# Optimization experiments

Measured on AMD Instinct MI355X. Metric: run time of the kernel, lower is better.

Reference implementation:

```python
import jax, jax.numpy as jnp
import numpy as np

B, T, C, H, N, L, V = 2, 512, 512, 8, 64, 12, 2560
DW, DA, DV, DG, F4 = 64, 64, 32, 128, 2048
GN_EPS = 64e-5  # torch GroupNorm eps = (1e-5)*head_size_divisor**2 with divisor 8


def _ln(x, w, b, eps=1e-5):
    m = x.mean(-1, keepdims=True)
    va = ((x - m) ** 2).mean(-1, keepdims=True)
    return (x - m) * jax.lax.rsqrt(va + eps) * w + b


def _group_norm(x, w, b):
    # GroupNorm(H groups) applied per token over each head's N channels
    xh = x.reshape(B, T, H, N)
    m = xh.mean(-1, keepdims=True)
    va = ((xh - m) ** 2).mean(-1, keepdims=True)
    return ((xh - m) * jax.lax.rsqrt(va + GN_EPS)).reshape(B, T, C) * w + b


def _time_shift(x):
    # ZeroPad2d((0,0,1,-1)): prepend zero step, drop last
    return jnp.pad(x, ((0, 0), (1, 0), (0, 0)))[:, :-1, :]


def _rwkv7_scan(r, w, k, v, a, b):
    # all inputs (B,T,H,N) float32; w already = exp(-exp(w_pre))
    def step(state, inp):
        r_t, w_t, k_t, v_t, a_t, b_t = inp  # (B,H,N)
        sa = jnp.einsum('bhij,bhj->bhi', state, a_t)  # S @ a (contract key dim)
        state = state * w_t[:, :, None, :] + sa[..., None] * b_t[:, :, None, :] + v_t[..., None] * k_t[:, :, None, :]
        return state, jnp.einsum('bhij,bhj->bhi', state, r_t)
    xs = tuple(jnp.moveaxis(t, 1, 0) for t in (r, w, k, v, a, b))  # (T,B,H,N)
    _, out = jax.lax.scan(step, jnp.zeros((B, H, N, N), jnp.float32), xs)
    return jnp.moveaxis(out, 0, 1)  # (B,T,H,N)


def _forward(tokens, emb, ln1_w, ln1_b, mx_r, mx_w, mx_k, mx_v, mx_a, mx_g,
             w0, w1, w2, a0, a1, a2, v0, v1, v2, g1, g2, k_k, k_a, r_k,
             Wr, Wk, Wv, Wo, gnx_w, gnx_b, ln2_w, ln2_b, Wfk, Wfv,
             lno_w, lno_b, Whead, bhead):
    hn = lambda t: t.reshape(B, T, H, N)
    x = emb[tokens]  # (B,T,C)
    v_first = x
    for i in range(L):
        # ---- RWKV-7 time-mix ----
        h = _ln(x, ln1_w[i], ln1_b[i])
        xx = _time_shift(h) - h
        xr = h + xx * mx_r[i]; xw = h + xx * mx_w[i]; xk = h + xx * mx_k[i]
        xv = h + xx * mx_v[i]; xa = h + xx * mx_a[i]; xg = h + xx * mx_g[i]
        r = xr @ Wr[i]
        wp = -jax.nn.softplus(-(w0[i] + jnp.tanh(xw @ w1[i]) @ w2[i])) - 0.5
        k = xk @ Wk[i]
        v = xv @ Wv[i]
        if i == 0:
            v_first = v
        else:
            v = v + (v_first - v) * jax.nn.sigmoid(v0[i] + (xv @ v1[i]) @ v2[i])
        a = jax.nn.sigmoid(a0[i] + (xa @ a1[i]) @ a2[i])
        g = jax.nn.sigmoid(xg @ g1[i]) @ g2[i]
        kk = hn(k * k_k[i])
        kk = (kk / jnp.maximum(jnp.linalg.norm(kk, axis=-1, keepdims=True), 1e-12)).reshape(B, T, C)
        k2 = k * (1.0 + (a - 1.0) * k_a[i])
        wdec = jnp.exp(-jnp.exp(wp.astype(jnp.float32)))
        y = _rwkv7_scan(hn(r).astype(jnp.float32), hn(wdec), hn(k2).astype(jnp.float32),
                        hn(v).astype(jnp.float32), hn(-kk).astype(jnp.float32),
                        hn(kk * a).astype(jnp.float32)).astype(x.dtype).reshape(B, T, C)
        y = _group_norm(y, gnx_w[i], gnx_b[i])
        y = y + ((hn(r) * hn(k2) * r_k[i].reshape(H, N)).sum(-1, keepdims=True) * hn(v)).reshape(B, T, C)
        x = x + (y * g) @ Wo[i]
        # ---- squared-ReLU channel-mix FFN (residual) ----
        h2 = _ln(x, ln2_w[i], ln2_b[i])
        x = x + jnp.square(jax.nn.relu(h2 @ Wfk[i])) @ Wfv[i]
    return _ln(x, lno_w, lno_b) @ Whead + bhead  # (B,T,V)


def setup_inputs():
    key = jax.random.key(0)
    ctr = [0]
    def nk():
        ctr[0] += 1
        return jax.random.fold_in(key, ctr[0])
    def nrm(shape, s=0.02):
        return jax.random.normal(nk(), shape, jnp.float32) * s
    def uni(shape):
        return jax.random.uniform(nk(), shape, dtype=jnp.float32)
    inp = {}
    inp['tokens'] = jax.random.randint(nk(), (B, T), 0, V, dtype=jnp.int32)
    inp['emb'] = nrm((V, C), 0.02)
    inp['ln1_w'] = jnp.ones((L, C)); inp['ln1_b'] = jnp.zeros((L, C))
    for nm in ('mx_r', 'mx_w', 'mx_k', 'mx_v', 'mx_a', 'mx_g'):
        inp[nm] = uni((L, C))
    inp['w0'] = nrm((L, C), 0.3) - 0.5
    inp['w1'] = nrm((L, C, DW)); inp['w2'] = nrm((L, DW, C), 0.1)
    inp['a0'] = nrm((L, C), 0.1); inp['a1'] = nrm((L, C, DA)); inp['a2'] = nrm((L, DA, C), 0.1)
    inp['v0'] = jnp.ones((L, C)); inp['v1'] = nrm((L, C, DV)); inp['v2'] = nrm((L, DV, C), 0.1)
    inp['g1'] = nrm((L, C, DG)); inp['g2'] = nrm((L, DG, C), 0.1)
    inp['k_k'] = 0.85 * jnp.ones((L, C)); inp['k_a'] = jnp.ones((L, C)); inp['r_k'] = nrm((L, C), 0.1)
    for nm in ('Wr', 'Wk', 'Wv', 'Wo'):
        inp[nm] = nrm((L, C, C), 0.02)
    inp['gnx_w'] = jnp.ones((L, C)); inp['gnx_b'] = jnp.zeros((L, C))
    inp['ln2_w'] = jnp.ones((L, C)); inp['ln2_b'] = jnp.zeros((L, C))
    inp['Wfk'] = nrm((L, C, F4), 0.02); inp['Wfv'] = nrm((L, F4, C), 0.02)
    inp['lno_w'] = jnp.ones((C,)); inp['lno_b'] = jnp.zeros((C,))
    inp['Whead'] = nrm((C, V), 0.02); inp['bhead'] = jnp.zeros((V,))
    return inp


def reference(tokens, emb, ln1_w, ln1_b, mx_r, mx_w, mx_k, mx_v, mx_a, mx_g,
              w0, w1, w2, a0, a1, a2, v0, v1, v2, g1, g2, k_k, k_a, r_k,
              Wr, Wk, Wv, Wo, gnx_w, gnx_b, ln2_w, ln2_b, Wfk, Wfv,
              lno_w, lno_b, Whead, bhead):
    return _forward(tokens, emb, ln1_w, ln1_b, mx_r, mx_w, mx_k, mx_v, mx_a, mx_g,
                    w0, w1, w2, a0, a1, a2, v0, v1, v2, g1, g2, k_k, k_a, r_k,
                    Wr, Wk, Wv, Wo, gnx_w, gnx_b, ln2_w, ln2_b, Wfk, Wfv,
                    lno_w, lno_b, Whead, bhead)
```

## Files before the change

### kernel.cpp

```cpp
#include <hip/hip_runtime.h>
#include <hip/hip_bf16.h>
#include <math.h>

#define Bq 2
#define Tq 512
#define Cq 512
#define Hq 8
#define Lq 12
#define Vq 2560
#define F4q 2048
#define BTq (Bq*Tq)

typedef float4 f4;
typedef __hip_bfloat16 bf16;
typedef __attribute__((ext_vector_type(8))) short bf16x8;
typedef __attribute__((ext_vector_type(4))) float f32x4;

static __device__ __forceinline__ float sigm(float x){ return 1.0f/(1.0f+expf(-x)); }
static __device__ __forceinline__ float splus(float x){ return fmaxf(x,0.0f) + log1pf(expf(-fabsf(x))); }
static __device__ __forceinline__ float b2f(short u){ unsigned int x = ((unsigned int)(unsigned short)u)<<16; float f; __builtin_memcpy(&f,&x,4); return f; }
static __device__ __forceinline__ short f2b(float f){ bf16 h = __float2bfloat16(f); unsigned short us; __builtin_memcpy(&us,&h,2); return (short)us; }

__device__ __forceinline__ void gload16(const void* gptr, void* lptr){
  __builtin_amdgcn_global_load_lds(
// ... 14 lines not shown
  int l = blockIdx.z;
  const float* s = src + (size_t)l*sstride;
  bf16* d = dst + (size_t)l*dstride;
  int n0 = blockIdx.x*32, k0 = blockIdx.y*32;
  int tx = threadIdx.x, ty = threadIdx.y;
  #pragma unroll
  for (int r=0;r<32;r+=8) tile[ty+r][tx] = s[(size_t)(k0+ty+r)*N + n0+tx];
  __syncthreads();
  #pragma unroll
  for (int r=0;r<32;r+=8) d[(size_t)(n0+ty+r)*K + k0+tx] = __float2bfloat16(tile[tx][ty+r]);
}

__global__ __launch_bounds__(256) void k_tr_split(const float* __restrict__ src,
    bf16* __restrict__ dhi, bf16* __restrict__ dlo,
    int K, int N, size_t sstride, size_t dstride){
  __shared__ float tile[32][33];
  int l = blockIdx.z;
  const float* s = src + (size_t)l*sstride;
  int n0 = blockIdx.x*32, k0 = blockIdx.y*32;
  int tx = threadIdx.x, ty = threadIdx.y;
  #pragma unroll
  for (int r=0;r<32;r+=8) tile[ty+r][tx] = s[(size_t)(k0+ty+r)*N + n0+tx];
  __syncthreads();
  #pragma unroll
  for (int r=0;r<32;r+=8){
    float v = tile[tx][ty+r];
    bf16 hv = __float2bfloat16(v);
    size_t idx = (size_t)l*dstride + (size_t)(n0+ty+r)*K + k0+tx;
    dhi[idx] = hv;
    dlo[idx] = __float2bfloat16(v - __bfloat162float(hv));
  }
}

__global__ __launch_bounds__(128) void k_ln(const float* __restrict__ x, const float* __restrict__ w,
    const float* __restrict__ b, float* __restrict__ o){
  int bt = blockIdx.x, tid = threadIdx.x;
  f4 v = ((const f4*)(x + (size_t)bt*Cq))[tid];
  float s = v.x+v.y+v.z+v.w;
  float q = v.x*v.x + v.y*v.y + v.z*v.z + v.w*v.w;
  #pragma unroll
  for (int m=1;m<64;m<<=1){ s += __shfl_xor(s,m); q += __shfl_xor(q,m); }
  __shared__ float ss[2], qs[2];
  if ((tid&63)==0){ ss[tid>>6]=s; qs[tid>>6]=q; }
  __syncthreads();
  s = ss[0]+ss[1]; q = qs[0]+qs[1];
  float mean = s*(1.0f/Cq);
  float inv = rsqrtf(q*(1.0f/Cq) - mean*mean + 1e-5f);
  f4 W = ((const f4*)w)[tid], Bb = ((const f4*)b)[tid];
  f4 r;
  r.x = (v.x-mean)*inv*W.x + Bb.x;
  r.y = (v.y-mean)*inv*W.y + Bb.y;
  r.z = (v.z-mean)*inv*W.z + Bb.z;
  r.w = (v.w-mean)*inv*W.w + Bb.w;
  ((f4*)(o + (size_t)bt*Cq))[tid] = r;
}

__global__ __launch_bounds__(128) void k_ln_split(const float* __restrict__ x, const float* __restrict__ w,
    const float* __restrict__ b, bf16* __restrict__ oh, bf16* __restrict__ ol){
  int bt = blockIdx.x, tid = threadIdx.x;
  f4 v = ((const f4*)(x + (size_t)bt*Cq))[tid];
  float s = v.x+v.y+v.z+v.w;
  float q = v.x*v.x + v.y*v.y + v.z*v.z + v.w*v.w;
  #pragma unroll
  for (int m=1;m<64;m<<=1){ s += __shfl_xor(s,m); q += __shfl_xor(q,m); }
  __shared__ float ss[2], qs[2];
  if ((tid&63)==0){ ss[tid>>6]=s; qs[tid>>6]=q; }
  __syncthreads();
  s = ss[0]+ss[1]; q = qs[0]+qs[1];
  float mean = s*(1.0f/Cq);
  float inv = rsqrtf(q*(1.0f/Cq) - mean*mean + 1e-5f);
  f4 W = ((const f4*)w)[tid], Bb = ((const f4*)b)[tid];
  float vv[4] = {(v.x-mean)*inv*W.x + Bb.x, (v.y-mean)*inv*W.y + Bb.y,
                 (v.z-mean)*inv*W.z + Bb.z, (v.w-mean)*inv*W.w + Bb.w};
  short4 hi, lo;
  short* hp = &hi.x; short* lp = &lo.x;
  #pragma unroll
  for (int u=0;u<4;u++){ hp[u] = f2b(vv[u]); lp[u] = f2b(vv[u] - b2f(hp[u])); }
  ((short4*)(oh + (size_t)bt*Cq))[tid] = hi;
  ((short4*)(ol + (size_t)bt*Cq))[tid] = lo;
}

__global__ __launch_bounds__(128) void k_ln_bf(const float* __restrict__ x, const float* __restrict__ w,
    const float* __restrict__ b, bf16* __restrict__ o){
  int bt = blockIdx.x, tid = threadIdx.x;
  f4 v = ((const f4*)(x + (size_t)bt*Cq))[tid];
  float s = v.x+v.y+v.z+v.w;
  float q = v.x*v.x + v.y*v.y + v.z*v.z + v.w*v.w;
  #pragma unroll
  for (int m=1;m<64;m<<=1){ s += __shfl_xor(s,m); q += __shfl_xor(q,m); }
  __shared__ float ss[2], qs[2];
  if ((tid&63)==0){ ss[tid>>6]=s; qs[tid>>6]=q; }
  __syncthreads();
  s = ss[0]+ss[1]; q = qs[0]+qs[1];
  float mean = s*(1.0f/Cq);
  float inv = rsqrtf(q*(1.0f/Cq) - mean*mean + 1e-5f);
  f4 W = ((const f4*)w)[tid], Bb = ((const f4*)b)[tid];
  short4 r;
  r.x = f2b((v.x-mean)*inv*W.x + Bb.x);
  r.y = f2b((v.y-mean)*inv*W.y + Bb.y);
  r.z = f2b((v.z-mean)*inv*W.z + Bb.z);
  r.w = f2b((v.w-mean)*inv*W.w + Bb.w);
  ((short4*)(o + (size_t)bt*Cq))[tid] = r;
}

__global__ __launch_bounds__(128) void k_mix_split(const float* __restrict__ h,
    const float* __restrict__ mr, const float* __restrict__ mw, const float* __restrict__ mk,
    const float* __restrict__ mv, const float* __restrict__ ma, const float* __restrict__ mg,
    bf16* __restrict__ xrh, bf16* __restrict__ xrl,
    bf16* __restrict__ xwh, bf16* __restrict__ xwl,
    bf16* __restrict__ xkh, bf16* __restrict__ xkl,
    bf16* __restrict__ xvh, bf16* __restrict__ xvl,
    bf16* __restrict__ xah, bf16* __restrict__ xal,
    bf16* __restrict__ xgh, bf16* __restrict__ xgl){
  int bt = blockIdx.x, tid = threadIdx.x;
  int t = bt & (Tq-1);
  f4 hc = ((const f4*)(h + (size_t)bt*Cq))[tid];
  f4 hp = make_float4(0.f,0.f,0.f,0.f);
  if (t) hp = ((const f4*)(h + (size_t)(bt-1)*Cq))[tid];
  float xxx = hp.x-hc.x, xxy = hp.y-hc.y, xxz = hp.z-hc.z, xxw = hp.w-hc.w;
  #define MIXS(dh, dl, m) { f4 M = ((const f4*)(m))[tid]; \
    float m0 = fmaf(xxx, M.x, hc.x), m1 = fmaf(xxy, M.y, hc.y); \
    float m2 = fmaf(xxz, M.z, hc.z), m3 = fmaf(xxw, M.w, hc.w); \
    short4 hi, lo; \
    hi.x = f2b(m0); lo.x = f2b(m0 - b2f(hi.x)); \
    hi.y = f2b(m1); lo.y = f2b(m1 - b2f(hi.y)); \
    hi.z = f2b(m2); lo.z = f2b(m2 - b2f(hi.z)); \
    hi.w = f2b(m3); lo.w = f2b(m3 - b2f(hi.w)); \
    ((short4*)((dh) + (size_t)bt*Cq))[tid] = hi; \
    ((short4*)((dl) + (size_t)bt*Cq))[tid] = lo; }
  MIXS(xrh, xrl, mr) MIXS(xwh, xwl, mw) MIXS(xkh, xkl, mk)
  MIXS(xvh, xvl, mv) MIXS(xah, xal, ma) MIXS(xgh, xgl, mg)
  #undef MIXS
}

template<int BM,int BN,int BK,int ACT,int OM>
__global__ __launch_bounds__(256) void k_sgemm(
    const bf16* __restrict__ Ah, const bf16* __restrict__ Al,
    const bf16* __restrict__ Bh, const bf16* __restrict__ Bl,
    void* __restrict__ Chv, bf16* __restrict__ Cl, int N, int K){
  constexpr int SWZ = (BK==64)?7:3;
  constexpr int ABYTES = BM*BK*2, BBYTES = BN*BK*2;
  __shared__ __align__(16) char lds[2][2*(ABYTES+BBYTES)];
  const int tid = threadIdx.x;
  const int w = tid>>6, ln = tid&63;
  const int wr = w>>1, wc = w&1;
  constexpr int WM = BM/2, WN = BN/2;
  constexpr int MR = WM/16, NR = WN/16;
  const int row0 = blockIdx.y*BM, col0 = blockIdx.x*BN;
  constexpr int LPR = BK/8;
  constexpr int RPC = 64/LPR;
  constexpr int CHA = BM/RPC, CHB = BN/RPC;
  const int srow = ln/LPR;
  const int kb  = (ln%LPR)*16;

  f32x4 acc[MR][NR];
  #pragma unroll
  for (int m=0;m<MR;m++)
    #pragma unroll
    for (int n=0;n<NR;n++)
      acc[m][n] = (f32x4){0.f,0.f,0.f,0.f};

  auto stage = [&](int buf, int k0){
    #pragma unroll
    for (int q=0;q<CHA/4;q++){
      int ch = w*(CHA/4)+q;
// ... 49 lines not shown
          acc[m][n] = __builtin_amdgcn_mfma_f32_16x16x32_bf16(ah[m], bh[n], acc[m][n], 0,0,0);
          acc[m][n] = __builtin_amdgcn_mfma_f32_16x16x32_bf16(ah[m], bl[n], acc[m][n], 0,0,0);
          acc[m][n] = __builtin_amdgcn_mfma_f32_16x16x32_bf16(al[m], bh[n], acc[m][n], 0,0,0);
        }
    }
    __syncthreads();
  }

  #pragma unroll
  for (int m=0;m<MR;m++){
    #pragma unroll
    for (int n=0;n<NR;n++){
      int col = col0 + wc*WN + n*16 + (ln&15);
      int rbase = row0 + wr*WM + m*16 + ((ln>>4)<<2);
      #pragma unroll
      for (int r=0;r<4;r++){
        float v = acc[m][n][r];
        if (ACT==1) v = tanhf(v);
        else if (ACT==2) v = sigm(v);
        else if (ACT==3){ v = fmaxf(v,0.f); v = v*v; }
        size_t o = (size_t)(rbase+r)*N + col;
        if (OM==0) ((float*)Chv)[o] = v;
        else if (OM==1) ((float*)Chv)[o] += v;
        else {
          bf16 hv = __float2bfloat16(v);
          ((bf16*)Chv)[o] = hv;
          Cl[o] = __float2bfloat16(v - __bfloat162float(hv));
        }
      }
    }
  }
}

template<int BM,int BN,int BK>
__global__ __launch_bounds__(256) void k_mgemm(const bf16* __restrict__ A,
    const bf16* __restrict__ Bt, const float* __restrict__ bias,
    float* __restrict__ Cm, int N, int K){
  constexpr int SWZ = (BK==64)?7:3;
  constexpr int ABYTES = BM*BK*2, BBYTES = BN*BK*2;
  __shared__ __align__(16) char lds[2][ABYTES+BBYTES];
  const int tid = threadIdx.x;
  const int w = tid>>6, ln = tid&63;
  const int wr = w>>1, wc = w&1;
  constexpr int WM = BM/2, WN = BN/2;
  constexpr int MR = WM/16, NR = WN/16;
  const int row0 = blockIdx.y*BM, col0 = blockIdx.x*BN;
  constexpr int LPR = BK/8;
  constexpr int RPC = 64/LPR;
  constexpr int CHA = BM/RPC, CHB = BN/RPC;
  const int srow = ln/LPR;
  const int kb  = (ln%LPR)*16;

  f32x4 acc[MR][NR];
  #pragma unroll
  for (int m=0;m<MR;m++)
    #pragma unroll
    for (int n=0;n<NR;n++)
      acc[m][n] = (f32x4){0.f,0.f,0.f,0.f};

  auto stage = [&](int buf, int k0){
    #pragma unroll
    for (int q=0;q<CHA/4;q++){
      int ch = w*(CHA/4)+q;
      int row = ch*RPC + srow;
      int kbs = kb ^ ((row&SWZ)<<4);
      gload16((const char*)(A + (size_t)(row0+row)*K + k0) + kbs, &lds[buf][ch*1024]);
// ... 56 lines not shown
    const float* __restrict__ vraw, const float* __restrict__ vfirst,
    const float* __restrict__ wpp, const float* __restrict__ aap, const float* __restrict__ vvp,
    const float* __restrict__ w0, const float* __restrict__ a0, const float* __restrict__ v0,
    const float* __restrict__ kkw, const float* __restrict__ kaw,
    float* __restrict__ scan_in, float* __restrict__ k2b, float* __restrict__ vb){
  int bt = blockIdx.x, hh = blockIdx.y, n = threadIdx.x;
  int c = (hh<<6) + n;
  size_t ic = (size_t)bt*Cq + c;
  int b = bt >> 9, t = bt & (Tq-1);
  float kvv = kb[ic];
  float kkq = kvv * kkw[c];
  float s = kkq*kkq;
  #pragma unroll
  for (int m=1;m<64;m<<=1) s += __shfl_xor(s,m);
  float kkn = kkq / fmaxf(sqrtf(s), 1e-12f);
  float aq = sigm(a0[c] + aap[ic]);
  float wvv = -splus(-(w0[c] + wpp[ic])) - 0.5f;
  float wd = expf(-expf(wvv));
  float vq;
  if (layer==0) vq = vfirst[ic];
  else { float vr = vraw[ic]; vq = fmaf(sigm(v0[c]+vvp[ic]), vfirst[ic]-vr, vr); }
  float k2q = kvv * fmaf(aq-1.0f, kaw[c], 1.0f);
  float* dst = scan_in + ((size_t)(b*Hq+hh)*Tq + t)*384;
  dst[n]       = rb[ic];
  dst[64+n]    = wd;
  dst[128+n]   = k2q;
  dst[192+n]   = vq;
  dst[256+n]   = -kkn;
  dst[320+n]   = kkn*aq;
  k2b[ic] = k2q;
  vb[ic]  = vq;
}

struct Step { float r[8], w[8], k[8], a[8], b[8], v; };

__device__ __forceinline__ void load_step(const float* __restrict__ st, int jc, int i, Step& s){
  *(f4*)&s.r[0] = *(const f4*)(st + jc);       *(f4*)&s.r[4] = *(const f4*)(st + jc + 4);
  *(f4*)&s.w[0] = *(const f4*)(st + 64 + jc);  *(f4*)&s.w[4] = *(const f4*)(st + 64 + jc + 4);
  *(f4*)&s.k[0] = *(const f4*)(st + 128 + jc); *(f4*)&s.k[4] = *(const f4*)(st + 128 + jc + 4);
  *(f4*)&s.a[0] = *(const f4*)(st + 256 + jc); *(f4*)&s.a[4] = *(const f4*)(st + 256 + jc + 4);
  *(f4*)&s.b[0] = *(const f4*)(st + 320 + jc); *(f4*)&s.b[4] = *(const f4*)(st + 320 + jc + 4);
  s.v = st[192 + i];
}

__device__ __forceinline__ float step_compute(float S[8], const Step& s){
  float sa0=0.f, sa1=0.f;
  #pragma unroll
  for (int u=0;u<4;u++){ sa0 = fmaf(S[u], s.a[u], sa0); sa1 = fmaf(S[u+4], s.a[u+4], sa1); }
  float sa = sa0+sa1;
  sa += __shfl_xor(sa,1); sa += __shfl_xor(sa,2); sa += __shfl_xor(sa,4);
  #pragma unroll
  for (int u=0;u<8;u++)
    S[u] = fmaf(s.v, s.k[u], fmaf(sa, s.b[u], S[u]*s.w[u]));
  float o0=0.f, o1=0.f;
  #pragma unroll
  for (int u=0;u<4;u++){ o0 = fmaf(S[u], s.r[u], o0); o1 = fmaf(S[u+4], s.r[u+4], o1); }
  float o = o0+o1;
  o += __shfl_xor(o,1); o += __shfl_xor(o,2); o += __shfl_xor(o,4);
  return o;
}

__global__ __launch_bounds__(64) void k_scan(const float* __restrict__ scan_in, float* __restrict__ y){
  int blk = blockIdx.x;
  int bh = blk>>3, w = blk&7;
  int lane = threadIdx.x;
  int il = lane>>3, c8 = lane&7, jc = c8<<3;
  int i = w*8 + il;
  int b = bh>>3, hh = bh&7;
  const float* base = scan_in + (size_t)bh*Tq*384;
  float* yrow = y + (size_t)b*Tq*Cq + (hh<<6) + i;
  float S[8];
  #pragma unroll
  for (int u=0;u<8;u++) S[u]=0.f;
  Step A_, B_;
  load_step(base, jc, i, A_);
  for (int t=0;t<Tq;t+=2){
    load_step(base + (size_t)(t+1)*384, jc, i, B_);
    float o = step_compute(S, A_);
    if (c8==0) yrow[(size_t)t*Cq] = o;
    if (t+2<Tq) load_step(base + (size_t)(t+2)*384, jc, i, A_);
    o = step_compute(S, B_);
    if (c8==0) yrow[(size_t)(t+1)*Cq] = o;
  }
}

__global__ __launch_bounds__(512) void k_post(const float* __restrict__ y,
    const float* __restrict__ rb, const float* __restrict__ k2b,
    const float* __restrict__ vb, const float* __restrict__ gb,
    const float* __restrict__ gnw, const float* __restrict__ gnb,
    const float* __restrict__ rk, bf16* __restrict__ zh, bf16* __restrict__ zl){
  int bt = blockIdx.x, c = threadIdx.x;
  size_t ic = (size_t)bt*Cq + c;
  float yv = y[ic];
  float s = yv, q = yv*yv;
  float rr = rb[ic]*k2b[ic]*rk[c];
  #pragma unroll
  for (int m=1;m<64;m<<=1){ s += __shfl_xor(s,m); q += __shfl_xor(q,m); rr += __shfl_xor(rr,m); }
  float mean = s*(1.0f/64.0f);
  float inv = rsqrtf(q*(1.0f/64.0f) - mean*mean + 64e-5f);
  float gn = (yv-mean)*inv*gnw[c] + gnb[c];
  float z = (gn + rr*vb[ic]) * gb[ic];
  bf16 hv = __float2bfloat16(z);
  zh[ic] = hv;
  zl[ic] = __float2bfloat16(z - __bfloat162float(hv));
}

extern "C" void kernel_launch(void* const* d_in, const int* in_sizes, int n_in,
                              void* d_out, int out_size, void* d_ws, size_t ws_size,
                              hipStream_t stream){
  const int*   tok  = (const int*)d_in[0];
  const float* emb  = (const float*)d_in[1];
  const float* ln1w = (const float*)d_in[2];
  const float* ln1b = (const float*)d_in[3];
  const float* mxr  = (const float*)d_in[4];
  const float* mxw  = (const float*)d_in[5];
// ... 5 lines not shown
  const float* w1   = (const float*)d_in[11];
  const float* w2   = (const float*)d_in[12];
  const float* a0   = (const float*)d_in[13];
  const float* a1   = (const float*)d_in[14];
  const float* a2   = (const float*)d_in[15];
  const float* v0   = (const float*)d_in[16];
  const float* v1   = (const float*)d_in[17];
  const float* v2   = (const float*)d_in[18];
  const float* g1   = (const float*)d_in[19];
  const float* g2   = (const float*)d_in[20];
  const float* kkw  = (const float*)d_in[21];
  const float* kaw  = (const float*)d_in[22];
  const float* rkw  = (const float*)d_in[23];
  const float* Wr   = (const float*)d_in[24];
  const float* Wk   = (const float*)d_in[25];
  const float* Wv   = (const float*)d_in[26];
  const float* Wo   = (const float*)d_in[27];
  const float* gnw  = (const float*)d_in[28];
  const float* gnb  = (const float*)d_in[29];
  const float* ln2w = (const float*)d_in[30];
  const float* ln2b = (const float*)d_in[31];
  const float* Wfk  = (const float*)d_in[32];
  const float* Wfv  = (const float*)d_in[33];
  const float* lnow = (const float*)d_in[34];
  const float* lnob = (const float*)d_in[35];
  const float* Whead= (const float*)d_in[36];
  const float* bhead= (const float*)d_in[37];
  float* out = (float*)d_out;

  float* ws = (float*)d_ws;
  size_t off = 0;
  const size_t BTC = (size_t)BTq*Cq;
  float* x      = ws + off; off += BTC;
  float* hf     = ws + off; off += BTC;
  float* rb     = ws + off; off += BTC;
  float* kb     = ws + off; off += BTC;
  float* vraw   = ws + off; off += BTC;
  float* vfirst = ws + off; off += BTC;
  float* wpp    = ws + off; off += BTC;
  float* aap    = ws + off; off += BTC;
  float* vvp    = ws + off; off += BTC;
  float* gbuf   = ws + off; off += BTC;
  float* k2b    = ws + off; off += BTC;
  float* vbuf   = ws + off; off += BTC;
  float* yb     = ws + off; off += BTC;
  float* scan_in= ws + off; off += (size_t)Bq*Hq*Tq*384;

  bf16* bp = (bf16*)(ws + off);
  size_t bo = 0;
  bf16* xrh = bp + bo; bo += BTC;  bf16* xrl = bp + bo; bo += BTC;
  bf16* xwh = bp + bo; bo += BTC;  bf16* xwl = bp + bo; bo += BTC;
  bf16* xkh = bp + bo; bo += BTC;  bf16* xkl = bp + bo; bo += BTC;
  bf16* xvh = bp + bo; bo += BTC;  bf16* xvl = bp + bo; bo += BTC;
  bf16* xah = bp + bo; bo += BTC;  bf16* xal = bp + bo; bo += BTC;
  bf16* xgh = bp + bo; bo += BTC;  bf16* xgl = bp + bo; bo += BTC;
  bf16* hh  = bp + bo; bo += BTC;  bf16* hl  = bp + bo; bo += BTC;
  bf16* zbh = bp + bo; bo += BTC;  bf16* zbl = bp + bo; bo += BTC;
  bf16* fkh = bp + bo; bo += (size_t)BTq*F4q;
  bf16* fkl = bp + bo; bo += (size_t)BTq*F4q;
  bf16* t1h = bp + bo; bo += (size_t)BTq*64;  bf16* t1l = bp + bo; bo += (size_t)BTq*64;
  bf16* t2h = bp + bo; bo += (size_t)BTq*64;  bf16* t2l = bp + bo; bo += (size_t)BTq*64;
  bf16* t3h = bp + bo; bo += (size_t)BTq*32;  bf16* t3l = bp + bo; bo += (size_t)BTq*32;
  bf16* t4h = bp + bo; bo += (size_t)BTq*128; bf16* t4l = bp + bo; bo += (size_t)BTq*128;
  const size_t CC = (size_t)Cq*Cq;
  bf16* WrTh = bp + bo; bo += Lq*CC;  bf16* WrTl = bp + bo; bo += Lq*CC;
  bf16* WkTh = bp + bo; bo += Lq*CC;  bf16* WkTl = bp + bo; bo += Lq*CC;
  bf16* WvTh = bp + bo; bo += Lq*CC;  bf16* WvTl = bp + bo; bo += Lq*CC;
  bf16* WoTh = bp + bo; bo += Lq*CC;  bf16* WoTl = bp + bo; bo += Lq*CC;
  const size_t C64 = (size_t)Cq*64, C32 = (size_t)Cq*32, C128 = (size_t)Cq*128;
  bf16* w1Th = bp + bo; bo += Lq*C64; bf16* w1Tl = bp + bo; bo += Lq*C64;
  bf16* w2Th = bp + bo; bo += Lq*C64; bf16* w2Tl = bp + bo; bo += Lq*C64;
  bf16* a1Th = bp + bo; bo += Lq*C64; bf16* a1Tl = bp + bo; bo += Lq*C64;
  bf16* a2Th = bp + bo; bo += Lq*C64; bf16* a2Tl = bp + bo; bo += Lq*C64;
  bf16* v1Th = bp + bo; bo += Lq*C32; bf16* v1Tl = bp + bo; bo += Lq*C32;
  bf16* v2Th = bp + bo; bo += Lq*C32; bf16* v2Tl = bp + bo; bo += Lq*C32;
  bf16* g1Th = bp + bo; bo += Lq*C128; bf16* g1Tl = bp + bo; bo += Lq*C128;
  bf16* g2Th = bp + bo; bo += Lq*C128; bf16* g2Tl = bp + bo; bo += Lq*C128;
  const size_t CF = (size_t)Cq*F4q;
  bf16* WfkTh = bp + bo; bo += CF;  bf16* WfkTl = bp + bo; bo += CF;
  bf16* WfvTh = bp + bo; bo += CF;  bf16* WfvTl = bp + bo; bo += CF;
  bf16* WhT   = bp + bo; bo += (size_t)Cq*Vq;

  dim3 tb(32,8);
  k_tr_split<<<dim3(16,16,Lq),tb,0,stream>>>(Wr, WrTh, WrTl, Cq, Cq, CC, CC);
  k_tr_split<<<dim3(16,16,Lq),tb,0,stream>>>(Wk, WkTh, WkTl, Cq, Cq, CC, CC);
  k_tr_split<<<dim3(16,16,Lq),tb,0,stream>>>(Wv, WvTh, WvTl, Cq, Cq, CC, CC);
  k_tr_split<<<dim3(16,16,Lq),tb,0,stream>>>(Wo, WoTh, WoTl, Cq, Cq, CC, CC);
  k_tr_split<<<dim3(2,16,Lq),tb,0,stream>>>(w1, w1Th, w1Tl, Cq, 64, C64, C64);
  k_tr_split<<<dim3(16,2,Lq),tb,0,stream>>>(w2, w2Th, w2Tl, 64, Cq, C64, C64);
  k_tr_split<<<dim3(2,16,Lq),tb,0,stream>>>(a1, a1Th, a1Tl, Cq, 64, C64, C64);
  k_tr_split<<<dim3(16,2,Lq),tb,0,stream>>>(a2, a2Th, a2Tl, 64, Cq, C64, C64);
  k_tr_split<<<dim3(1,16,Lq),tb,0,stream>>>(v1, v1Th, v1Tl, Cq, 32, C32, C32);
  k_tr_split<<<dim3(16,1,Lq),tb,0,stream>>>(v2, v2Th, v2Tl, 32, Cq, C32, C32);
  k_tr_split<<<dim3(4,16,Lq),tb,0,stream>>>(g1, g1Th, g1Tl, Cq, 128, C128, C128);
  k_tr_split<<<dim3(16,4,Lq),tb,0,stream>>>(g2, g2Th, g2Tl, 128, Cq, C128, C128);
  k_tr<<<dim3(80,16,1),tb,0,stream>>>(Whead, WhT, Cq, Vq, 0, 0);

  k_embed<<<BTq,128,0,stream>>>(tok, emb, x);

  dim3 gC(Cq/64, BTq/64);
  dim3 g64(1, BTq/64);
  dim3 g32(1, BTq/64);
  dim3 g128(2, BTq/64);
  dim3 gF(F4q/64, BTq/64);
  dim3 gH(Vq/64, BTq/64);

  for (int l=0;l<Lq;l++){
    size_t lc = (size_t)l*Cq;
    k_ln<<<BTq,128,0,stream>>>(x, ln1w+lc, ln1b+lc, hf);
    k_mix_split<<<BTq,128,0,stream>>>(hf, mxr+lc, mxw+lc, mxk+lc, mxv+lc, mxa+lc, mxg+lc,
                                      xrh,xrl, xwh,xwl, xkh,xkl, xvh,xvl, xah,xal, xgh,xgl);
    k_sgemm<64,64,64,0,0><<<gC,256,0,stream>>>(xrh, xrl, WrTh+l*CC, WrTl+l*CC, rb, nullptr, Cq, Cq);
    k_sgemm<64,64,64,0,0><<<gC,256,0,stream>>>(xkh, xkl, WkTh+l*CC, WkTl+l*CC, kb, nullptr, Cq, Cq);
    k_sgemm<64,64,64,0,0><<<gC,256,0,stream>>>(xvh, xvl, WvTh+l*CC, WvTl+l*CC,
                                               (l==0 ? vfirst : vraw), nullptr, Cq, Cq);
    k_sgemm<64,64,64,1,2><<<g64,256,0,stream>>>(xwh, xwl, w1Th+l*C64, w1Tl+l*C64, t1h, t1l, 64, Cq);
    k_sgemm<64,64,64,0,0><<<gC,256,0,stream>>>(t1h, t1l, w2Th+l*C64, w2Tl+l*C64, wpp, nullptr, Cq, 64);
    k_sgemm<64,64,64,0,2><<<g64,256,0,stream>>>(xah, xal, a1Th+l*C64, a1Tl+l*C64, t2h, t2l, 64, Cq);
    k_sgemm<64,64,64,0,0><<<gC,256,0,stream>>>(t2h, t2l, a2Th+l*C64, a2Tl+l*C64, aap, nullptr, Cq, 64);
    if (l > 0){
      k_sgemm<64,32,64,0,2><<<g32,256,0,stream>>>(xvh, xvl, v1Th+l*C32, v1Tl+l*C32, t3h, t3l, 32, Cq);
      k_sgemm<64,64,32,0,0><<<gC,256,0,stream>>>(t3h, t3l, v2Th+l*C32, v2Tl+l*C32, vvp, nullptr, Cq, 32);
    }
    k_sgemm<64,64,64,2,2><<<g128,256,0,stream>>>(xgh, xgl, g1Th+l*C128, g1Tl+l*C128, t4h, t4l, 128, Cq);
    k_sgemm<64,64,64,0,0><<<gC,256,0,stream>>>(t4h, t4l, g2Th+l*C128, g2Tl+l*C128, gbuf, nullptr, Cq, 128);
    k_prescan<<<dim3(BTq,Hq),64,0,stream>>>(l, rb, kb, vraw, vfirst, wpp, aap, vvp,
                                            w0+lc, a0+lc, v0+lc, kkw+lc, kaw+lc,
                                            scan_in, k2b, vbuf);
    k_scan<<<Bq*Hq*8,64,0,stream>>>(scan_in, yb);
    k_post<<<BTq,512,0,stream>>>(yb, rb, k2b, vbuf, gbuf, gnw+lc, gnb+lc, rkw+lc, zbh, zbl);
    k_sgemm<64,64,64,0,1><<<gC,256,0,stream>>>(zbh, zbl, WoTh+l*CC, WoTl+l*CC, x, nullptr, Cq, Cq);
    k_ln_split<<<BTq,128,0,stream>>>(x, ln2w+lc, ln2b+lc, hh, hl);
    k_tr_split<<<dim3(64,16,1),tb,0,stream>>>(Wfk + l*CF, WfkTh, WfkTl, Cq, F4q, 0, 0);
    k_tr_split<<<dim3(16,64,1),tb,0,stream>>>(Wfv + l*CF, WfvTh, WfvTl, F4q, Cq, 0, 0);
    k_sgemm<64,64,64,3,2><<<gF,256,0,stream>>>(hh, hl, WfkTh, WfkTl, fkh, fkl, F4q, Cq);
    k_sgemm<64,64,64,0,1><<<gC,256,0,stream>>>(fkh, fkl, WfvTh, WfvTl, x, nullptr, Cq, F4q);
  }
  k_ln_bf<<<BTq,128,0,stream>>>(x, lnow, lnob, hh);
  k_mgemm<64,64,64><<<gH,256,0,stream>>>(hh, WhT, bhead, out, Vq, Cq);
}
```

Before: 4.625 ms.

## Fuse LayerNorm with token mix, batch projection GEMMs, widen scan parallelism

Merges the first LayerNorm into the time-shift mix kernel. It recomputes the previous token's normalization so the intermediate fp32 buffer is no longer written and read back. The r/k/v projections and the two stages of LoRA-style low-rank GEMMs are grouped into three batched launches indexed by blockIdx.z, which cuts launch count and fills more CUs per launch. The scan kernel now splits each head's state over 16 blocks with 4 state columns per lane and a deeper prefetch, doubling the block count. The cost is a small amount of redundant LN work, padded wasted tiles in the grouped GEMMs, and the v1 low-rank GEMM now running on layer 0 too.

```diff
diff --git a/kernel.cpp b/kernel.cpp
--- a/kernel.cpp
+++ b/kernel.cpp
@@ -70,27 +70,59 @@
   }
 }
 
-__global__ __launch_bounds__(128) void k_ln(const float* __restrict__ x, const float* __restrict__ w,
-    const float* __restrict__ b, float* __restrict__ o){
+__global__ __launch_bounds__(128) void k_lnmix(const float* __restrict__ x,
+    const float* __restrict__ lw, const float* __restrict__ lb,
+    const float* __restrict__ mr, const float* __restrict__ mw, const float* __restrict__ mk,
+    const float* __restrict__ mv, const float* __restrict__ ma, const float* __restrict__ mg,
+    bf16* __restrict__ xrh, bf16* __restrict__ xrl,
+    bf16* __restrict__ xwh, bf16* __restrict__ xwl,
+    bf16* __restrict__ xkh, bf16* __restrict__ xkl,
+    bf16* __restrict__ xvh, bf16* __restrict__ xvl,
+    bf16* __restrict__ xah, bf16* __restrict__ xal,
+    bf16* __restrict__ xgh, bf16* __restrict__ xgl){
   int bt = blockIdx.x, tid = threadIdx.x;
-  f4 v = ((const f4*)(x + (size_t)bt*Cq))[tid];
-  float s = v.x+v.y+v.z+v.w;
-  float q = v.x*v.x + v.y*v.y + v.z*v.z + v.w*v.w;
-  #pragma unroll
-  for (int m=1;m<64;m<<=1){ s += __shfl_xor(s,m); q += __shfl_xor(q,m); }
-  __shared__ float ss[2], qs[2];
-  if ((tid&63)==0){ ss[tid>>6]=s; qs[tid>>6]=q; }
+  int t = bt & (Tq-1);
+  f4 vc = ((const f4*)(x + (size_t)bt*Cq))[tid];
+  f4 vp = make_float4(0.f,0.f,0.f,0.f);
+  if (t) vp = ((const f4*)(x + (size_t)(bt-1)*Cq))[tid];
+  float sc = vc.x+vc.y+vc.z+vc.w;
+  float qc = vc.x*vc.x+vc.y*vc.y+vc.z*vc.z+vc.w*vc.w;
+  float sp = vp.x+vp.y+vp.z+vp.w;
+  float qp = vp.x*vp.x+vp.y*vp.y+vp.z*vp.z+vp.w*vp.w;
+  #pragma unroll
+  for (int m=1;m<64;m<<=1){
+    sc += __shfl_xor(sc,m); qc += __shfl_xor(qc,m);
+    sp += __shfl_xor(sp,m); qp += __shfl_xor(qp,m);
+  }
+  __shared__ float sh[4][2];
+  if ((tid&63)==0){ int w=tid>>6; sh[0][w]=sc; sh[1][w]=qc; sh[2][w]=sp; sh[3][w]=qp; }
   __syncthreads();
-  s = ss[0]+ss[1]; q = qs[0]+qs[1];
-  float mean = s*(1.0f/Cq);
-  float inv = rsqrtf(q*(1.0f/Cq) - mean*mean + 1e-5f);
-  f4 W = ((const f4*)w)[tid], Bb = ((const f4*)b)[tid];
-  f4 r;
-  r.x = (v.x-mean)*inv*W.x + Bb.x;
-  r.y = (v.y-mean)*inv*W.y + Bb.y;
-  r.z = (v.z-mean)*inv*W.z + Bb.z;
-  r.w = (v.w-mean)*inv*W.w + Bb.w;
-  ((f4*)(o + (size_t)bt*Cq))[tid] = r;
+  sc = sh[0][0]+sh[0][1]; qc = sh[1][0]+sh[1][1];
+  sp = sh[2][0]+sh[2][1]; qp = sh[3][0]+sh[3][1];
+  float mc = sc*(1.0f/Cq), ic = rsqrtf(qc*(1.0f/Cq)-mc*mc+1e-5f);
+  float mp = sp*(1.0f/Cq), ip = rsqrtf(qp*(1.0f/Cq)-mp*mp+1e-5f);
+  f4 W = ((const f4*)lw)[tid], Bb = ((const f4*)lb)[tid];
+  float hcx = (vc.x-mc)*ic*W.x+Bb.x, hcy = (vc.y-mc)*ic*W.y+Bb.y;
+  float hcz = (vc.z-mc)*ic*W.z+Bb.z, hcw = (vc.w-mc)*ic*W.w+Bb.w;
+  float hpx=0.f, hpy=0.f, hpz=0.f, hpw=0.f;
+  if (t){
+    hpx = (vp.x-mp)*ip*W.x+Bb.x; hpy = (vp.y-mp)*ip*W.y+Bb.y;
+    hpz = (vp.z-mp)*ip*W.z+Bb.z; hpw = (vp.w-mp)*ip*W.w+Bb.w;
+  }
+  float xxx = hpx-hcx, xxy = hpy-hcy, xxz = hpz-hcz, xxw = hpw-hcw;
+  #define MIXS(dh, dl, m) { f4 M = ((const f4*)(m))[tid]; \
+    float m0 = fmaf(xxx, M.x, hcx), m1 = fmaf(xxy, M.y, hcy); \
+    float m2 = fmaf(xxz, M.z, hcz), m3 = fmaf(xxw, M.w, hcw); \
+    short4 hi, lo; \
+    hi.x = f2b(m0); lo.x = f2b(m0 - b2f(hi.x)); \
+    hi.y = f2b(m1); lo.y = f2b(m1 - b2f(hi.y)); \
+    hi.z = f2b(m2); lo.z = f2b(m2 - b2f(hi.z)); \
+    hi.w = f2b(m3); lo.w = f2b(m3 - b2f(hi.w)); \
+    ((short4*)((dh) + (size_t)bt*Cq))[tid] = hi; \
+    ((short4*)((dl) + (size_t)bt*Cq))[tid] = lo; }
+  MIXS(xrh, xrl, mr) MIXS(xwh, xwl, mw) MIXS(xkh, xkl, mk)
+  MIXS(xvh, xvl, mv) MIXS(xah, xal, ma) MIXS(xgh, xgl, mg)
+  #undef MIXS
 }
 
 __global__ __launch_bounds__(128) void k_ln_split(const float* __restrict__ x, const float* __restrict__ w,
@@ -139,36 +171,6 @@
   r.z = f2b((v.z-mean)*inv*W.z + Bb.z);
   r.w = f2b((v.w-mean)*inv*W.w + Bb.w);
   ((short4*)(o + (size_t)bt*Cq))[tid] = r;
-}
-
-__global__ __launch_bounds__(128) void k_mix_split(const float* __restrict__ h,
-    const float* __restrict__ mr, const float* __restrict__ mw, const float* __restrict__ mk,
-    const float* __restrict__ mv, const float* __restrict__ ma, const float* __restrict__ mg,
-    bf16* __restrict__ xrh, bf16* __restrict__ xrl,
-    bf16* __restrict__ xwh, bf16* __restrict__ xwl,
-    bf16* __restrict__ xkh, bf16* __restrict__ xkl,
-    bf16* __restrict__ xvh, bf16* __restrict__ xvl,
-    bf16* __restrict__ xah, bf16* __restrict__ xal,
-    bf16* __restrict__ xgh, bf16* __restrict__ xgl){
-  int bt = blockIdx.x, tid = threadIdx.x;
-  int t = bt & (Tq-1);
-  f4 hc = ((const f4*)(h + (size_t)bt*Cq))[tid];
-  f4 hp = make_float4(0.f,0.f,0.f,0.f);
-  if (t) hp = ((const f4*)(h + (size_t)(bt-1)*Cq))[tid];
-  float xxx = hp.x-hc.x, xxy = hp.y-hc.y, xxz = hp.z-hc.z, xxw = hp.w-hc.w;
-  #define MIXS(dh, dl, m) { f4 M = ((const f4*)(m))[tid]; \
-    float m0 = fmaf(xxx, M.x, hc.x), m1 = fmaf(xxy, M.y, hc.y); \
-    float m2 = fmaf(xxz, M.z, hc.z), m3 = fmaf(xxw, M.w, hc.w); \
-    short4 hi, lo; \
-    hi.x = f2b(m0); lo.x = f2b(m0 - b2f(hi.x)); \
-    hi.y = f2b(m1); lo.y = f2b(m1 - b2f(hi.y)); \
-    hi.z = f2b(m2); lo.z = f2b(m2 - b2f(hi.z)); \
-    hi.w = f2b(m3); lo.w = f2b(m3 - b2f(hi.w)); \
-    ((short4*)((dh) + (size_t)bt*Cq))[tid] = hi; \
-    ((short4*)((dl) + (size_t)bt*Cq))[tid] = lo; }
-  MIXS(xrh, xrl, mr) MIXS(xwh, xwl, mw) MIXS(xkh, xkl, mk)
-  MIXS(xvh, xvl, mv) MIXS(xah, xal, ma) MIXS(xgh, xgl, mg)
-  #undef MIXS
 }
 
 template<int BM,int BN,int BK,int ACT,int OM>
@@ -284,6 +286,134 @@
   }
 }
 
+struct SBatch {
+  const bf16* Ah[4]; const bf16* Al[4];
+  const bf16* Bh[4]; const bf16* Bl[4];
+  void* Ch[4]; bf16* Cl[4];
+  int N[4]; int K[4]; int act[4];
+};
+
+template<int BM,int BN,int BK,int OM>
+__global__ __launch_bounds__(256) void k_sgemm_b(SBatch p){
+  const int z = blockIdx.z;
+  const int N = p.N[z], K = p.K[z], act = p.act[z];
+  const int col0 = blockIdx.x*BN;
+  if (col0 >= N) return;
+  const bf16* __restrict__ Ah = p.Ah[z];
+  const bf16* __restrict__ Al = p.Al[z];
+  const bf16* __restrict__ Bh = p.Bh[z];
+  const bf16* __restrict__ Bl = p.Bl[z];
+  void* Chv = p.Ch[z];
+  bf16* Cl = p.Cl[z];
+  constexpr int SWZ = (BK==64)?7:3;
+  constexpr int ABYTES = BM*BK*2, BBYTES = BN*BK*2;
+  __shared__ __align__(16) char lds[2][2*(ABYTES+BBYTES)];
+  const int tid = threadIdx.x;
+  const int w = tid>>6, ln = tid&63;
+  const int wr = w>>1, wc = w&1;
+  constexpr int WM = BM/2, WN = BN/2;
+  constexpr int MR = WM/16, NR = WN/16;
+  const int row0 = blockIdx.y*BM;
+  constexpr int LPR = BK/8;
+  constexpr int RPC = 64/LPR;
+  constexpr int CHA = BM/RPC, CHB = BN/RPC;
+  const int srow = ln/LPR;
+  const int kb  = (ln%LPR)*16;
+
+  f32x4 acc[MR][NR];
+  #pragma unroll
+  for (int m=0;m<MR;m++)
+    #pragma unroll
+    for (int n=0;n<NR;n++)
+      acc[m][n] = (f32x4){0.f,0.f,0.f,0.f};
+
+  auto stage = [&](int buf, int k0){
+    #pragma unroll
+    for (int q=0;q<CHA/4;q++){
+      int ch = w*(CHA/4)+q;
+      int row = ch*RPC + srow;
+      int kbs = kb ^ ((row&SWZ)<<4);
+      size_t go = (size_t)(row0+row)*K + k0;
+      gload16((const char*)(Ah+go)+kbs, &lds[buf][ch*1024]);
+      gload16((const char*)(Al+go)+kbs, &lds[buf][ABYTES + ch*1024]);
+    }
+    #pragma unroll
+    for (int q=0;q<CHB/4;q++){
+      int ch = w*(CHB/4)+q;
+      int row = ch*RPC + srow;
+      int kbs = kb ^ ((row&SWZ)<<4);
+      size_t go = (size_t)(col0+row)*K + k0;
+      gload16((const char*)(Bh+go)+kbs, &lds[buf][2*ABYTES + ch*1024]);
+      gload16((const char*)(Bl+go)+kbs, &lds[buf][2*ABYTES+BBYTES + ch*1024]);
+    }
+  };
+
+  stage(0, 0);
+  __syncthreads();
+  const int nt = K/BK;
+  for (int t=0;t<nt;t++){
+    int buf = t&1;
+    if (t+1<nt) stage(buf^1, (t+1)*BK);
+    const char* Lah = &lds[buf][0];
+    const char* Lal = &lds[buf][ABYTES];
+    const char* Lbh = &lds[buf][2*ABYTES];
+    const char* Lbl = &lds[buf][2*ABYTES+BBYTES];
+    #pragma unroll
+    for (int kk=0;kk<BK/32;kk++){
+      bf16x8 ah[MR], al[MR], bh[NR], bl[NR];
+      int klo = kk*64 + ((ln>>4)<<4);
+      #pragma unroll
+      for (int m=0;m<MR;m++){
+        int row = wr*WM + m*16 + (ln&15);
+        int off = row*(BK*2) + (klo ^ ((row&SWZ)<<4));
+        ah[m] = *(const bf16x8*)(Lah + off);
+        al[m] = *(const bf16x8*)(Lal + off);
+      }
+      #pragma unroll
+      for (int n=0;n<NR;n++){
+        int row = wc*WN + n*16 + (ln&15);
+        int off = row*(BK*2) + (klo ^ ((row&SWZ)<<4));
+        bh[n] = *(const bf16x8*)(Lbh + off);
+        bl[n] = *(const bf16x8*)(Lbl + off);
+      }
+      #pragma unroll
+      for (int m=0;m<MR;m++)
+        #pragma unroll
+        for (int n=0;n<NR;n++){
+          acc[m][n] = __builtin_amdgcn_mfma_f32_16x16x32_bf16(ah[m], bh[n], acc[m][n], 0,0,0);
+          acc[m][n] = __builtin_amdgcn_mfma_f32_16x16x32_bf16(ah[m], bl[n], acc[m][n], 0,0,0);
+          acc[m][n] = __builtin_amdgcn_mfma_f32_16x16x32_bf16(al[m], bh[n], acc[m][n], 0,0,0);
+        }
+    }
+    __syncthreads();
+  }
+
+  #pragma unroll
+  for (int m=0;m<MR;m++){
+    #pragma unroll
+    for (int n=0;n<NR;n++){
+      int col = col0 + wc*WN + n*16 + (ln&15);
+      if (col >= N) continue;
+      int rbase = row0 + wr*WM + m*16 + ((ln>>4)<<2);
+      #pragma unroll
+      for (int r=0;r<4;r++){
+        float v = acc[m][n][r];
+        if (act==1) v = tanhf(v);
+        else if (act==2) v = sigm(v);
+        else if (act==3){ v = fmaxf(v,0.f); v = v*v; }
+        size_t o = (size_t)(rbase+r)*N + col;
+        if (OM==0) ((float*)Chv)[o] = v;
+        else if (OM==1) ((float*)Chv)[o] += v;
+        else {
+          bf16 hv = __float2bfloat16(v);
+          ((bf16*)Chv)[o] = hv;
+          Cl[o] = __float2bfloat16(v - __bfloat162float(hv));
+        }
+      }
+    }
+  }
+}
+
 template<int BM,int BN,int BK>
 __global__ __launch_bounds__(256) void k_mgemm(const bf16* __restrict__ A,
     const bf16* __restrict__ Bt, const float* __restrict__ bias,
@@ -406,55 +536,61 @@
   vb[ic]  = vq;
 }
 
-struct Step { float r[8], w[8], k[8], a[8], b[8], v; };
-
-__device__ __forceinline__ void load_step(const float* __restrict__ st, int jc, int i, Step& s){
-  *(f4*)&s.r[0] = *(const f4*)(st + jc);       *(f4*)&s.r[4] = *(const f4*)(st + jc + 4);
-  *(f4*)&s.w[0] = *(const f4*)(st + 64 + jc);  *(f4*)&s.w[4] = *(const f4*)(st + 64 + jc + 4);
-  *(f4*)&s.k[0] = *(const f4*)(st + 128 + jc); *(f4*)&s.k[4] = *(const f4*)(st + 128 + jc + 4);
-  *(f4*)&s.a[0] = *(const f4*)(st + 256 + jc); *(f4*)&s.a[4] = *(const f4*)(st + 256 + jc + 4);
-  *(f4*)&s.b[0] = *(const f4*)(st + 320 + jc); *(f4*)&s.b[4] = *(const f4*)(st + 320 + jc + 4);
+struct Step4 { float r[4], w[4], k[4], a[4], b[4], v; };
+
+__device__ __forceinline__ void load_step4(const float* __restrict__ st, int jc, int i, Step4& s){
+  *(f4*)&s.r[0] = *(const f4*)(st + jc);
+  *(f4*)&s.w[0] = *(const f4*)(st + 64 + jc);
+  *(f4*)&s.k[0] = *(const f4*)(st + 128 + jc);
+  *(f4*)&s.a[0] = *(const f4*)(st + 256 + jc);
+  *(f4*)&s.b[0] = *(const f4*)(st + 320 + jc);
   s.v = st[192 + i];
 }
 
-__device__ __forceinline__ float step_compute(float S[8], const Step& s){
-  float sa0=0.f, sa1=0.f;
-  #pragma unroll
-  for (int u=0;u<4;u++){ sa0 = fmaf(S[u], s.a[u], sa0); sa1 = fmaf(S[u+4], s.a[u+4], sa1); }
-  float sa = sa0+sa1;
-  sa += __shfl_xor(sa,1); sa += __shfl_xor(sa,2); sa += __shfl_xor(sa,4);
-  #pragma unroll
-  for (int u=0;u<8;u++)
+__device__ __forceinline__ float step_compute4(float S[4], const Step4& s){
+  float sa = 0.f;
+  #pragma unroll
+  for (int u=0;u<4;u++) sa = fmaf(S[u], s.a[u], sa);
+  sa += __shfl_xor(sa,1); sa += __shfl_xor(sa,2);
+  sa += __shfl_xor(sa,4); sa += __shfl_xor(sa,8);
+  #pragma unroll
+  for (int u=0;u<4;u++)
     S[u] = fmaf(s.v, s.k[u], fmaf(sa, s.b[u], S[u]*s.w[u]));
-  float o0=0.f, o1=0.f;
-  #pragma unroll
-  for (int u=0;u<4;u++){ o0 = fmaf(S[u], s.r[u], o0); o1 = fmaf(S[u+4], s.r[u+4], o1); }
-  float o = o0+o1;
-  o += __shfl_xor(o,1); o += __shfl_xor(o,2); o += __shfl_xor(o,4);
+  float o = 0.f;
+  #pragma unroll
+  for (int u=0;u<4;u++) o = fmaf(S[u], s.r[u], o);
+  o += __shfl_xor(o,1); o += __shfl_xor(o,2);
+  o += __shfl_xor(o,4); o += __shfl_xor(o,8);
   return o;
 }
 
 __global__ __launch_bounds__(64) void k_scan(const float* __restrict__ scan_in, float* __restrict__ y){
   int blk = blockIdx.x;
-  int bh = blk>>3, w = blk&7;
+  int bh = blk>>4, w = blk&15;
   int lane = threadIdx.x;
-  int il = lane>>3, c8 = lane&7, jc = c8<<3;
-  int i = w*8 + il;
+  int il = lane>>4, c16 = lane&15, jc = c16<<2;
+  int i = w*4 + il;
   int b = bh>>3, hh = bh&7;
   const float* base = scan_in + (size_t)bh*Tq*384;
   float* yrow = y + (size_t)b*Tq*Cq + (hh<<6) + i;
-  float S[8];
-  #pragma unroll
-  for (int u=0;u<8;u++) S[u]=0.f;
-  Step A_, B_;
-  load_step(base, jc, i, A_);
-  for (int t=0;t<Tq;t+=2){
-    load_step(base + (size_t)(t+1)*384, jc, i, B_);
-    float o = step_compute(S, A_);
-    if (c8==0) yrow[(size_t)t*Cq] = o;
-    if (t+2<Tq) load_step(base + (size_t)(t+2)*384, jc, i, A_);
-    o = step_compute(S, B_);
-    if (c8==0) yrow[(size_t)(t+1)*Cq] = o;
+  float S[4] = {0.f,0.f,0.f,0.f};
+  Step4 P0,P1,P2,P3;
+  load_step4(base,      jc,i,P0);
+  load_step4(base+384,  jc,i,P1);
+  load_step4(base+768,  jc,i,P2);
+  for (int t=0;t<Tq;t+=4){
+    if (t+3<Tq) load_step4(base+(size_t)(t+3)*384, jc,i,P3);
+    float o = step_compute4(S,P0);
+    if (c16==0) yrow[(size_t)t*Cq] = o;
+    if (t+4<Tq) load_step4(base+(size_t)(t+4)*384, jc,i,P0);
+    o = step_compute4(S,P1);
+    if (c16==0) yrow[(size_t)(t+1)*Cq] = o;
+    if (t+5<Tq) load_step4(base+(size_t)(t+5)*384, jc,i,P1);
+    o = step_compute4(S,P2);
+    if (c16==0) yrow[(size_t)(t+2)*Cq] = o;
+    if (t+6<Tq) load_step4(base+(size_t)(t+6)*384, jc,i,P2);
+    o = step_compute4(S,P3);
+    if (c16==0) yrow[(size_t)(t+3)*Cq] = o;
   }
 }
 
@@ -526,7 +662,6 @@
   size_t off = 0;
   const size_t BTC = (size_t)BTq*Cq;
   float* x      = ws + off; off += BTC;
-  float* hf     = ws + off; off += BTC;
   float* rb     = ws + off; off += BTC;
   float* kb     = ws + off; off += BTC;
   float* vraw   = ws + off; off += BTC;
@@ -566,7 +701,7 @@
   bf16* w2Th = bp + bo; bo += Lq*C64; bf16* w2Tl = bp + bo; bo += Lq*C64;
   bf16* a1Th = bp + bo; bo += Lq*C64; bf16* a1Tl = bp + bo; bo += Lq*C64;
   bf16* a2Th = bp + bo; bo += Lq*C64; bf16* a2Tl = bp + bo; bo += Lq*C64;
-  bf16* v1Th = bp + bo; bo += Lq*C32; bf16* v1Tl = bp + bo; bo += Lq*C32;
+  bf16* v1Th = bp + bo; bo += Lq*C64; bf16* v1Tl = bp + bo; bo += Lq*C64;
   bf16* v2Th = bp + bo; bo += Lq*C32; bf16* v2Tl = bp + bo; bo += Lq*C32;
   bf16* g1Th = bp + bo; bo += Lq*C128; bf16* g1Tl = bp + bo; bo += Lq*C128;
   bf16* g2Th = bp + bo; bo += Lq*C128; bf16* g2Tl = bp + bo; bo += Lq*C128;
@@ -584,7 +719,7 @@
   k_tr_split<<<dim3(16,2,Lq),tb,0,stream>>>(w2, w2Th, w2Tl, 64, Cq, C64, C64);
   k_tr_split<<<dim3(2,16,Lq),tb,0,stream>>>(a1, a1Th, a1Tl, Cq, 64, C64, C64);
   k_tr_split<<<dim3(16,2,Lq),tb,0,stream>>>(a2, a2Th, a2Tl, 64, Cq, C64, C64);
-  k_tr_split<<<dim3(1,16,Lq),tb,0,stream>>>(v1, v1Th, v1Tl, Cq, 32, C32, C32);
+  k_tr_split<<<dim3(1,16,Lq),tb,0,stream>>>(v1, v1Th, v1Tl, Cq, 32, C32, C64);
   k_tr_split<<<dim3(16,1,Lq),tb,0,stream>>>(v2, v2Th, v2Tl, 32, Cq, C32, C32);
   k_tr_split<<<dim3(4,16,Lq),tb,0,stream>>>(g1, g1Th, g1Tl, Cq, 128, C128, C128);
   k_tr_split<<<dim3(16,4,Lq),tb,0,stream>>>(g2, g2Th, g2Tl, 128, Cq, C128, C128);
@@ -593,35 +728,43 @@
   k_embed<<<BTq,128,0,stream>>>(tok, emb, x);
 
   dim3 gC(Cq/64, BTq/64);
-  dim3 g64(1, BTq/64);
-  dim3 g32(1, BTq/64);
-  dim3 g128(2, BTq/64);
   dim3 gF(F4q/64, BTq/64);
   dim3 gH(Vq/64, BTq/64);
 
   for (int l=0;l<Lq;l++){
     size_t lc = (size_t)l*Cq;
-    k_ln<<<BTq,128,0,stream>>>(x, ln1w+lc, ln1b+lc, hf);
-    k_mix_split<<<BTq,128,0,stream>>>(hf, mxr+lc, mxw+lc, mxk+lc, mxv+lc, mxa+lc, mxg+lc,
-                                      xrh,xrl, xwh,xwl, xkh,xkl, xvh,xvl, xah,xal, xgh,xgl);
-    k_sgemm<64,64,64,0,0><<<gC,256,0,stream>>>(xrh, xrl, WrTh+l*CC, WrTl+l*CC, rb, nullptr, Cq, Cq);
-    k_sgemm<64,64,64,0,0><<<gC,256,0,stream>>>(xkh, xkl, WkTh+l*CC, WkTl+l*CC, kb, nullptr, Cq, Cq);
-    k_sgemm<64,64,64,0,0><<<gC,256,0,stream>>>(xvh, xvl, WvTh+l*CC, WvTl+l*CC,
-                                               (l==0 ? vfirst : vraw), nullptr, Cq, Cq);
-    k_sgemm<64,64,64,1,2><<<g64,256,0,stream>>>(xwh, xwl, w1Th+l*C64, w1Tl+l*C64, t1h, t1l, 64, Cq);
-    k_sgemm<64,64,64,0,0><<<gC,256,0,stream>>>(t1h, t1l, w2Th+l*C64, w2Tl+l*C64, wpp, nullptr, Cq, 64);
-    k_sgemm<64,64,64,0,2><<<g64,256,0,stream>>>(xah, xal, a1Th+l*C64, a1Tl+l*C64, t2h, t2l, 64, Cq);
-    k_sgemm<64,64,64,0,0><<<gC,256,0,stream>>>(t2h, t2l, a2Th+l*C64, a2Tl+l*C64, aap, nullptr, Cq, 64);
-    if (l > 0){
-      k_sgemm<64,32,64,0,2><<<g32,256,0,stream>>>(xvh, xvl, v1Th+l*C32, v1Tl+l*C32, t3h, t3l, 32, Cq);
-      k_sgemm<64,64,32,0,0><<<gC,256,0,stream>>>(t3h, t3l, v2Th+l*C32, v2Tl+l*C32, vvp, nullptr, Cq, 32);
-    }
-    k_sgemm<64,64,64,2,2><<<g128,256,0,stream>>>(xgh, xgl, g1Th+l*C128, g1Tl+l*C128, t4h, t4l, 128, Cq);
-    k_sgemm<64,64,64,0,0><<<gC,256,0,stream>>>(t4h, t4l, g2Th+l*C128, g2Tl+l*C128, gbuf, nullptr, Cq, 128);
+    k_lnmix<<<BTq,128,0,stream>>>(x, ln1w+lc, ln1b+lc,
+                                  mxr+lc, mxw+lc, mxk+lc, mxv+lc, mxa+lc, mxg+lc,
+                                  xrh,xrl, xwh,xwl, xkh,xkl, xvh,xvl, xah,xal, xgh,xgl);
+    {
+      SBatch p{};
+      p.Ah[0]=xrh; p.Al[0]=xrl; p.Bh[0]=WrTh+l*CC; p.Bl[0]=WrTl+l*CC; p.Ch[0]=rb;
+      p.Ah[1]=xkh; p.Al[1]=xkl; p.Bh[1]=WkTh+l*CC; p.Bl[1]=WkTl+l*CC; p.Ch[1]=kb;
+      p.Ah[2]=xvh; p.Al[2]=xvl; p.Bh[2]=WvTh+l*CC; p.Bl[2]=WvTl+l*CC; p.Ch[2]=(l==0?vfirst:vraw);
+      for (int z=0;z<3;z++){ p.N[z]=Cq; p.K[z]=Cq; p.act[z]=0; p.Cl[z]=nullptr; }
+      k_sgemm_b<64,64,64,0><<<dim3(Cq/64, BTq/64, 3),256,0,stream>>>(p);
+    }
+    {
+      SBatch p{};
+      p.Ah[0]=xwh; p.Al[0]=xwl; p.Bh[0]=w1Th+l*C64;  p.Bl[0]=w1Tl+l*C64;  p.Ch[0]=t1h; p.Cl[0]=t1l; p.N[0]=64;  p.K[0]=Cq; p.act[0]=1;
+      p.Ah[1]=xah; p.Al[1]=xal; p.Bh[1]=a1Th+l*C64;  p.Bl[1]=a1Tl+l*C64;  p.Ch[1]=t2h; p.Cl[1]=t2l; p.N[1]=64;  p.K[1]=Cq; p.act[1]=0;
+      p.Ah[2]=xvh; p.Al[2]=xvl; p.Bh[2]=v1Th+l*C64;  p.Bl[2]=v1Tl+l*C64;  p.Ch[2]=t3h; p.Cl[2]=t3l; p.N[2]=32;  p.K[2]=Cq; p.act[2]=0;
+      p.Ah[3]=xgh; p.Al[3]=xgl; p.Bh[3]=g1Th+l*C128; p.Bl[3]=g1Tl+l*C128; p.Ch[3]=t4h; p.Cl[3]=t4l; p.N[3]=128; p.K[3]=Cq; p.act[3]=2;
+      k_sgemm_b<64,64,64,2><<<dim3(2, BTq/64, 4),256,0,stream>>>(p);
+    }
+    {
+      SBatch p{};
+      p.Ah[0]=t1h; p.Al[0]=t1l; p.Bh[0]=w2Th+l*C64;  p.Bl[0]=w2Tl+l*C64;  p.Ch[0]=wpp;  p.N[0]=Cq; p.K[0]=64;  p.act[0]=0;
+      p.Ah[1]=t2h; p.Al[1]=t2l; p.Bh[1]=a2Th+l*C64;  p.Bl[1]=a2Tl+l*C64;  p.Ch[1]=aap;  p.N[1]=Cq; p.K[1]=64;  p.act[1]=0;
+      p.Ah[2]=t3h; p.Al[2]=t3l; p.Bh[2]=v2Th+l*C32;  p.Bl[2]=v2Tl+l*C32;  p.Ch[2]=vvp;  p.N[2]=Cq; p.K[2]=32;  p.act[2]=0;
+      p.Ah[3]=t4h; p.Al[3]=t4l; p.Bh[3]=g2Th+l*C128; p.Bl[3]=g2Tl+l*C128; p.Ch[3]=gbuf; p.N[3]=Cq; p.K[3]=128; p.act[3]=0;
+      for (int z=0;z<4;z++) p.Cl[z]=nullptr;
+      k_sgemm_b<64,64,32,0><<<dim3(Cq/64, BTq/64, 4),256,0,stream>>>(p);
+    }
     k_prescan<<<dim3(BTq,Hq),64,0,stream>>>(l, rb, kb, vraw, vfirst, wpp, aap, vvp,
                                             w0+lc, a0+lc, v0+lc, kkw+lc, kaw+lc,
                                             scan_in, k2b, vbuf);
-    k_scan<<<Bq*Hq*8,64,0,stream>>>(scan_in, yb);
+    k_scan<<<Bq*Hq*16,64,0,stream>>>(scan_in, yb);
     k_post<<<BTq,512,0,stream>>>(yb, rb, k2b, vbuf, gbuf, gnw+lc, gnb+lc, rkw+lc, zbh, zbl);
     k_sgemm<64,64,64,0,1><<<gC,256,0,stream>>>(zbh, zbl, WoTh+l*CC, WoTl+l*CC, x, nullptr, Cq, Cq);
     k_ln_split<<<BTq,128,0,stream>>>(x, ln2w+lc, ln2b+lc, hh, hl);
```

New measurement: 3.869 ms. 1.2x faster.
